# Kernel tuning notes

Hardware: AMD Instinct MI355X
Metric: run time of the kernel (lower is better)

## Reference

```python
import jax, jax.numpy as jnp
import numpy as np

B, T, D = 32, 512, 384
DUR_MAX = 8          # durations drawn from [0, DUR_MAX)
MAX_LEN = T * (DUR_MAX - 1)  # 3584, static pad length (= target_mel_len)


def setup_inputs() -> dict:
    key = jax.random.key(0)
    kx, kd = jax.random.split(key)
    x = jax.random.normal(kx, (B, T, D), dtype=jnp.float32)
    duration_target = jax.random.randint(kd, (B, T), 0, DUR_MAX, dtype=jnp.int64)
    return {"x": x, "duration_target": duration_target, "target_mel_len": MAX_LEN}


def reference(x, duration_target, target_mel_len):
    # Effective duration: original does vec.expand(max(int(d), 1), -1),
    # so zero durations still produce one frame.
    eff = jnp.maximum(duration_target, 1)          # [B, T]
    cum = jnp.cumsum(eff, axis=1)                   # [B, T] exclusive upper bounds
    mel_len = cum[:, -1]                            # [B]
    L = int(target_mel_len)                         # static pad length
    frames = jnp.arange(L)                          # [L]
    # frame j belongs to phoneme i where cum[i-1] <= j < cum[i]
    idx = jax.vmap(lambda c: jnp.searchsorted(c, frames, side="right"))(cum)  # [B, L]
    idx = jnp.minimum(idx, x.shape[1] - 1)          # clamp padded region
    out = jnp.take_along_axis(x, idx[:, :, None], axis=1)  # [B, L, D]
    mask = frames[None, :] < mel_len[:, None]       # [B, L]
    out = out * mask[:, :, None].astype(out.dtype)  # zero padding like F.pad
    return out, mel_len.astype(jnp.int64)
```

## Files before the change

### kernel.cpp

```cpp
#include <hip/hip_runtime.h>


#define B_DIM 32
#define T_DIM 512
#define D_DIM 384
#define L_DIM 3584
#define VEC 96
#define RPB 8
#define CHUNKS (T_DIM / RPB)
#define BLOCKS (B_DIM * CHUNKS)

typedef float f32x4 __attribute__((ext_vector_type(4)));

__global__ void __launch_bounds__(256)
lr_fused(const f32x4* __restrict__ x, const int* __restrict__ dur,
         f32x4* __restrict__ out, float* __restrict__ mel_out) {
    const int blk  = blockIdx.x;
    const int b    = blk >> 6;
    const int c    = blk & 63;
    const int t    = threadIdx.x;
    const int lane = t & 63;
    const int wv   = t >> 6;

    const int2 dd = ((const int2*)(dur + b * T_DIM))[t];
    const int e0 = dd.x > 1 ? dd.x : 1;
    const int e1 = dd.y > 1 ? dd.y : 1;

    int val = e0 + e1;
    #pragma unroll
    for (int off = 1; off < 64; off <<= 1) {
        int n = __shfl_up(val, off, 64);
        if (lane >= off) val += n;
    }

    __shared__ int wsum[4];
    __shared__ int scum[T_DIM];
    if (lane == 63) wsum[wv] = val;
    __syncthreads();

    int base = 0, tot = 0;
    #pragma unroll
    for (int i = 0; i < 4; ++i) {
        int w = wsum[i];
        tot += w;
        if (i < wv) base += w;
    }
    const int c1 = val + base;
    scum[2 * t]     = c1 - e1;
    scum[2 * t + 1] = c1;
    __syncthreads();

    const int mel = tot;
    if (c == 0 && t == 0)
        mel_out[b] = (float)mel;

    const int r0 = c * RPB;
    const f32x4* xb   = x + (size_t)(b * T_DIM + r0) * VEC;
    f32x4*       outb = out + (size_t)b * L_DIM * VEC;

    #pragma unroll
    for (int i = 0; i < 3; ++i) {
        const int v = t + i * 256;
        const int r = v / VEC;
        const int w = v - r * VEC;
        const f32x4 xv = xb[v];
        const int gr = r0 + r;
        const int ce = scum[gr];
        const int cs = (gr == 0) ? 0 : scum[gr - 1];
        f32x4* o = outb + (size_t)cs * VEC + w;
        for (int k = cs; k < ce; ++k) {
            *o = xv;
            o += VEC;
        }
    }

    const int tailspan = L_DIM - mel;
    const int lo = mel + ((tailspan * c) >> 6);
    const int hi = mel + ((tailspan * (c + 1)) >> 6);
    const int n4 = (hi - lo) * VEC;
    const f32x4 z = (f32x4)0.f;
    f32x4* ob = outb + (size_t)lo * VEC;
    for (int v = t; v < n4; v += 256)
        ob[v] = z;
}

extern "C" void kernel_launch(void* const* d_in, const int* in_sizes, int n_in,
                              void* d_out, int out_size, void* d_ws, size_t ws_size,
                              hipStream_t stream) {
    const float* x   = (const float*)d_in[0];
    const int*   dur = (const int*)d_in[1];

    float* out     = (float*)d_out;
    float* mel_out = out + (size_t)B_DIM * L_DIM * D_DIM;

    lr_fused<<<dim3(BLOCKS), dim3(256), 0, stream>>>(
        (const f32x4*)x, dur, (f32x4*)out, mel_out);
}
```

Before: 193.5 us.

## Switch length regulator from input-row scatter to output-frame gather

Each block now owns a fixed 128-frame slice of the output instead of 8 input phonemes. Each thread writes the phoneme index for its frames into a shared lookup table, then the block gathers x rows (or zeros) and writes its slice contiguously. This removes the load imbalance of variable-length per-thread scatter loops and the separate tail-zeroing pass. In exchange, x rows are read repeatedly, once per output frame rather than once per phoneme, and the index table is filled by serial per-thread loops.

```diff
diff --git a/kernel.cpp b/kernel.cpp
--- a/kernel.cpp
+++ b/kernel.cpp
@@ -6,9 +6,11 @@
 #define D_DIM 384
 #define L_DIM 3584
 #define VEC 96
-#define RPB 8
-#define CHUNKS (T_DIM / RPB)
-#define BLOCKS (B_DIM * CHUNKS)
+#define F_PB 128
+#define CPB (L_DIM / F_PB)
+#define BLOCKS (B_DIM * CPB)
+#define F4_PB (F_PB * VEC)
+#define ITERS (F4_PB / 256)
 
 typedef float f32x4 __attribute__((ext_vector_type(4)));
 
@@ -16,8 +18,9 @@
 lr_fused(const f32x4* __restrict__ x, const int* __restrict__ dur,
          f32x4* __restrict__ out, float* __restrict__ mel_out) {
     const int blk  = blockIdx.x;
-    const int b    = blk >> 6;
-    const int c    = blk & 63;
+    const int b    = blk / CPB;
+    const int c    = blk - b * CPB;
+    const int f0   = c * F_PB;
     const int t    = threadIdx.x;
     const int lane = t & 63;
     const int wv   = t >> 6;
@@ -34,8 +37,9 @@
     }
 
     __shared__ int wsum[4];
-    __shared__ int scum[T_DIM];
+    __shared__ int sidx[F_PB];
     if (lane == 63) wsum[wv] = val;
+    if (t < F_PB) sidx[t] = -1;
     __syncthreads();
 
     int base = 0, tot = 0;
@@ -45,43 +49,38 @@
         tot += w;
         if (i < wv) base += w;
     }
-    const int c1 = val + base;
-    scum[2 * t]     = c1 - e1;
-    scum[2 * t + 1] = c1;
+    const int cum1 = val + base;
+    const int cum0 = cum1 - e1;
+    const int prev = cum0 - e0;
+
+    const int f1 = f0 + F_PB;
+    {
+        int lo = prev > f0 ? prev : f0;
+        int hi = cum0 < f1 ? cum0 : f1;
+        for (int f = lo; f < hi; ++f) sidx[f - f0] = 2 * t;
+        lo = cum0 > f0 ? cum0 : f0;
+        hi = cum1 < f1 ? cum1 : f1;
+        for (int f = lo; f < hi; ++f) sidx[f - f0] = 2 * t + 1;
+    }
     __syncthreads();
 
-    const int mel = tot;
     if (c == 0 && t == 0)
-        mel_out[b] = (float)mel;
+        mel_out[b] = (float)tot;
 
-    const int r0 = c * RPB;
-    const f32x4* xb   = x + (size_t)(b * T_DIM + r0) * VEC;
-    f32x4*       outb = out + (size_t)b * L_DIM * VEC;
+    const f32x4* xb = x + (size_t)b * T_DIM * VEC;
+    f32x4*       ob = out + ((size_t)b * L_DIM + f0) * VEC;
 
-    #pragma unroll
-    for (int i = 0; i < 3; ++i) {
-        const int v = t + i * 256;
-        const int r = v / VEC;
-        const int w = v - r * VEC;
-        const f32x4 xv = xb[v];
-        const int gr = r0 + r;
-        const int ce = scum[gr];
-        const int cs = (gr == 0) ? 0 : scum[gr - 1];
-        f32x4* o = outb + (size_t)cs * VEC + w;
-        for (int k = cs; k < ce; ++k) {
-            *o = xv;
-            o += VEC;
-        }
+    #pragma unroll 8
+    for (int i = 0; i < ITERS; ++i) {
+        const int v  = t + i * 256;
+        const int fl = v / VEC;
+        const int w  = v - fl * VEC;
+        const int id = sidx[fl];
+        f32x4 r = (f32x4)0.f;
+        if (id >= 0)
+            r = xb[id * VEC + w];
+        ob[v] = r;
     }
-
-    const int tailspan = L_DIM - mel;
-    const int lo = mel + ((tailspan * c) >> 6);
-    const int hi = mel + ((tailspan * (c + 1)) >> 6);
-    const int n4 = (hi - lo) * VEC;
-    const f32x4 z = (f32x4)0.f;
-    f32x4* ob = outb + (size_t)lo * VEC;
-    for (int v = t; v < n4; v += 256)
-        ob[v] = z;
 }
 
 extern "C" void kernel_launch(void* const* d_in, const int* in_sizes, int n_in,
```

After: 212.8 us. +10.0%, slower.
